# Optimization experiments

Hardware: AMD Instinct MI355X
Metric: run time of the kernel (lower is better)

The kernel has to match this reference:

```python
import jax, jax.numpy as jnp
import numpy as np

N_NODES = 100000
N_EDGES = 1600000
D = 128


def _gconv(x, edge_index, edge_weight, W, Wloop, b):
    # support = x @ W ; out = adj @ support + x @ Wloop + b
    support = x @ W                                   # [N, D]
    src, dst = edge_index[0], edge_index[1]
    msgs = support[src] * edge_weight[:, None]        # [E, D] gather (irregular)
    agg = jax.ops.segment_sum(msgs, dst, num_segments=x.shape[0])  # [N, D] scatter
    return agg + x @ Wloop + b


def setup_inputs() -> dict:
    key = jax.random.key(0)
    ks = jax.random.split(key, 9)
    s = 1.0 / np.sqrt(D)
    x = jax.random.normal(ks[0], (N_NODES, D), dtype=jnp.float32)
    edge_index = jax.random.randint(ks[1], (2, N_EDGES), 0, N_NODES, dtype=jnp.int32)
    edge_weight = jax.random.uniform(ks[2], (N_EDGES,), dtype=jnp.float32)
    W1 = jax.random.normal(ks[3], (D, D), dtype=jnp.float32) * s
    Wloop1 = jax.random.normal(ks[4], (D, D), dtype=jnp.float32) * s
    b1 = jax.random.normal(ks[5], (D,), dtype=jnp.float32) * 0.01
    W2 = jax.random.normal(ks[6], (D, D), dtype=jnp.float32) * s
    Wloop2 = jax.random.normal(ks[7], (D, D), dtype=jnp.float32) * s
    b2 = jax.random.normal(ks[8], (D,), dtype=jnp.float32) * 0.01
    return {"x": x, "edge_index": edge_index, "edge_weight": edge_weight,
            "W1": W1, "Wloop1": Wloop1, "b1": b1,
            "W2": W2, "Wloop2": Wloop2, "b2": b2}


def reference(x, edge_index, edge_weight, W1, Wloop1, b1, W2, Wloop2, b2):
    h = _gconv(x, edge_index, edge_weight, W1, Wloop1, b1)
    h = _gconv(h, edge_index, edge_weight, W2, Wloop2, b2)
    return (x + h) * 0.5
```

## Files before the change

kernel.cpp:

```cpp
#include <hip/hip_runtime.h>
#include <hip/hip_bf16.h>
#include <stdint.h>

#define D 128
#define BM 64
#define NB_BITS 9
#define NPB (1 << NB_BITS)
#define BCAP 10240
#define C3_EPB 4096

typedef __attribute__((ext_vector_type(8))) short bf16x8;
typedef __attribute__((ext_vector_type(4))) short short4_t;
typedef __attribute__((ext_vector_type(4))) float f32x4;
typedef unsigned int uint32;

static __device__ __forceinline__ short f2bf(float f) {
  uint32_t u = __builtin_bit_cast(uint32_t, f);
  u += 0x7fffu + ((u >> 16) & 1u);
  return (short)(u >> 16);
}

static __device__ __forceinline__ uint32 pk2bf(float a, float b) {
  return ((uint32)(unsigned short)f2bf(b) << 16) | (uint32)(unsigned short)f2bf(a);
}


__global__ void k_prep(const float* __restrict__ W1, const float* __restrict__ Wl1,
                       const float* __restrict__ W2, const float* __restrict__ Wl2,
                       short* __restrict__ BT1, short* __restrict__ BT2,
                       int* __restrict__ bcur) {
  int idx = blockIdx.x * 256 + threadIdx.x;
  if (idx < 2 * D * D) {
    int n = idx >> 7, k = idx & (D - 1);
    float v = (n < D) ? W1[k * D + n] : Wl1[k * D + (n - D)];
    BT1[idx] = f2bf(v);
  } else if (idx < 4 * D * D) {
    int i2 = idx - 2 * D * D;
    int n = i2 >> 7, k = i2 & (D - 1);
    float v = (n < D) ? W2[k * D + n] : Wl2[k * D + (n - D)];
    BT2[i2] = f2bf(v);
  } else if (idx < 4 * D * D + 256) {
    bcur[idx - 4 * D * D] = 0;
  }
}


__global__ __launch_bounds__(256) void k_bucket(const int* __restrict__ src,
                                                const int* __restrict__ dst,
                                                const float* __restrict__ wgt,
                                                int* __restrict__ bcur,
                                                int4* __restrict__ rec,
                                                int E, int nb) {
  __shared__ int lhist[256];
  __shared__ int lbase[256];
  const int t = threadIdx.x;
  const int e0 = blockIdx.x * C3_EPB;
  if (t < nb) lhist[t] = 0;
  __syncthreads();
  for (int i = t; i < C3_EPB; i += 256) {
    int e = e0 + i;
    if (e < E) atomicAdd(&lhist[dst[e] >> NB_BITS], 1);
  }
  __syncthreads();
  if (t < nb) {
    lbase[t] = atomicAdd(&bcur[t], lhist[t]);
    lhist[t] = 0;
  }
  __syncthreads();
  for (int i = t; i < C3_EPB; i += 256) {
    int e = e0 + i;
    if (e < E) {
      int d = dst[e];
      int b = d >> NB_BITS;
      int r = lbase[b] + atomicAdd(&lhist[b], 1);
      if (r >= BCAP) r = BCAP - 1;
      rec[(size_t)b * BCAP + r] =
          make_int4(src[e], __builtin_bit_cast(int, wgt[e]), d, 0);
    }
  }
}


__global__ __launch_bounds__(256) void k_sort(const int4* __restrict__ rec,
                                              const int* __restrict__ bcur,
                                              int* __restrict__ off,
                                              int2* __restrict__ pairs,
                                              int N, int nb) {
  __shared__ int bc[256];
  __shared__ int psum[256];
  __shared__ int lofs[NPB];
  const int t = threadIdx.x;
  const int b = blockIdx.x;

  int mycnt = (t < nb) ? min(bcur[t], BCAP) : 0;
  bc[t] = mycnt;
  __syncthreads();
  for (int dd = 1; dd < 256; dd <<= 1) {
    int a = (t >= dd) ? bc[t - dd] : 0;
    __syncthreads();
    bc[t] += a;
    __syncthreads();
  }
  const int cntb = min(bcur[b], BCAP);
  const int ebase = bc[b] - cntb;
  const int total = bc[nb - 1];
  const size_t rbase = (size_t)b * BCAP;
  const int n0 = b << NB_BITS;
  const int nn = min(NPB, N - n0);

  for (int i = t; i < NPB; i += 256) lofs[i] = 0;
  __syncthreads();
  for (int i = t; i < cntb; i += 256)
    atomicAdd(&lofs[rec[rbase + i].z & (NPB - 1)], 1);
  __syncthreads();

  int v0 = lofs[2 * t], v1 = lofs[2 * t + 1];
  int sum = v0 + v1;
  psum[t] = sum;
  __syncthreads();
  for (int dd = 1; dd < 256; dd <<= 1) {
    int a = (t >= dd) ? psum[t - dd] : 0;
    __syncthreads();
    psum[t] += a;
    __syncthreads();
  }
  int run = psum[t] - sum;
  lofs[2 * t] = run;
  lofs[2 * t + 1] = run + v0;
  __syncthreads();

  for (int i = t; i < nn; i += 256) off[n0 + i] = ebase + lofs[i];
  if (b == nb - 1 && t == 0) off[N] = total;
  __syncthreads();

  for (int i = t; i < cntb; i += 256) {
    int4 rr = rec[rbase + i];
    int r = atomicAdd(&lofs[rr.z & (NPB - 1)], 1);
    pairs[ebase + r] = make_int2(rr.x, rr.y);
  }
}


template<bool ABF16, bool IBF16, bool RESID>
__global__ __launch_bounds__(256) void k_gemm(const void* __restrict__ Ap,
                                              const short* __restrict__ BT,
                                              const float* __restrict__ bias,
                                              const float* __restrict__ resid,
                                              unsigned short* __restrict__ support,
                                              void* __restrict__ initp, int M) {
  __shared__ short As[BM * D];
  const int t = threadIdx.x;
  const int l = t & 63;
  const int w = t >> 6;
  const int lm = l & 15;
  const int lg = l >> 4;
  const int m0 = blockIdx.x * BM;
  const bool full = (m0 + BM <= M);

  short4_t aregs[8];
  float4 aregf[8];
#pragma unroll
  for (int i = 0; i < 8; ++i) {
    int id = t + i * 256;
    int row = id >> 5, c4 = id & 31;
    int gr = m0 + row; if (gr >= M) gr = M - 1;
    if (ABF16) aregs[i] = *(const short4_t*)((const short*)Ap + (size_t)gr * D + c4 * 4);
    else       aregf[i] = *(const float4*)((const float*)Ap + (size_t)gr * D + c4 * 4);
  }

  bf16x8 bfrag[4][4];
  const int colbase = w * 64 + lm;
#pragma unroll
  for (int cf = 0; cf < 4; ++cf) {
    const short* p = BT + (colbase + cf * 16) * D + lg * 8;
#pragma unroll
    for (int ks = 0; ks < 4; ++ks) bfrag[cf][ks] = *(const bf16x8*)(p + ks * 32);
  }

#pragma unroll
  for (int i = 0; i < 8; ++i) {
    int id = t + i * 256;
    int row = id >> 5, c4 = id & 31;
    short4_t s4;
    if (ABF16) s4 = aregs[i];
    else {
      float4 v = aregf[i];
      s4[0] = f2bf(v.x); s4[1] = f2bf(v.y); s4[2] = f2bf(v.z); s4[3] = f2bf(v.w);
    }
    int sidx = row * D + ((c4 * 4) ^ ((row & 7) << 3));
    *(short4_t*)(As + sidx) = s4;
  }
  __syncthreads();

  f32x4 acc[4][4] = {};
#pragma unroll
  for (int ks = 0; ks < 4; ++ks) {
    bf16x8 afrag[4];
    int kcol = ks * 32 + lg * 8;
#pragma unroll
    for (int rf = 0; rf < 4; ++rf) {
      int row = rf * 16 + lm;
      afrag[rf] = *(const bf16x8*)(As + row * D + (kcol ^ ((row & 7) << 3)));
    }
#pragma unroll
    for (int rf = 0; rf < 4; ++rf)
#pragma unroll
      for (int cf = 0; cf < 4; ++cf)
        acc[rf][cf] = __builtin_amdgcn_mfma_f32_16x16x32_bf16(
            bfrag[cf][ks], afrag[rf], acc[rf][cf], 0, 0, 0);
  }

  const bool isInit = (w >= 2);
  const int wcol = (w & 1) * 64;

  if (!isInit) {
#pragma unroll
    for (int rf = 0; rf < 4; ++rf) {
      int m = m0 + rf * 16 + lm;
#pragma unroll
      for (int cf = 0; cf < 4; ++cf) {
        int nb = wcol + cf * 16 + lg * 4;
        f32x4 a = acc[rf][cf];
        uint2 pk = make_uint2(pk2bf(a[0], a[1]), pk2bf(a[2], a[3]));
        if (full || m < M)
          *(uint2*)((uint32*)support + (size_t)m * 64 + (nb >> 1)) = pk;
      }
    }
  } else {
    float4 bv4[4];
#pragma unroll
    for (int cf = 0; cf < 4; ++cf)
      bv4[cf] = *(const float4*)(bias + wcol + cf * 16 + lg * 4);
#pragma unroll
    for (int rf = 0; rf < 4; ++rf) {
      int m = m0 + rf * 16 + lm;
      bool ok = full || m < M;
#pragma unroll
      for (int cf = 0; cf < 4; ++cf) {
        int nb = wcol + cf * 16 + lg * 4;
        f32x4 a = acc[rf][cf];
        float4 v;
        v.x = a[0] + bv4[cf].x; v.y = a[1] + bv4[cf].y;
        v.z = a[2] + bv4[cf].z; v.w = a[3] + bv4[cf].w;
        if (RESID) {
          if (ok) {
            float4 xr = *(const float4*)(resid + (size_t)m * D + nb);
            v.x = (v.x + xr.x) * 0.5f; v.y = (v.y + xr.y) * 0.5f;
            v.z = (v.z + xr.z) * 0.5f; v.w = (v.w + xr.w) * 0.5f;
          }
        }
        if (ok) {
          if (IBF16) {
            uint2 pk = make_uint2(pk2bf(v.x, v.y), pk2bf(v.z, v.w));
            *(uint2*)((uint32*)initp + (size_t)m * 64 + (nb >> 1)) = pk;
          } else {
            *(float4*)((float*)initp + (size_t)m * D + nb) = v;
          }
        }
      }
    }
  }
}


template<int MODE>
__global__ __launch_bounds__(256) void k_agg(const uint32* __restrict__ sup,
                                             const int* __restrict__ off,
                                             const int2* __restrict__ pairs,
                                             void* __restrict__ iop, int N) {
  int node = blockIdx.x * 4 + (threadIdx.x >> 6);
  if (node >= N) return;
  const int l = threadIdx.x & 63;
  const int beg = __builtin_amdgcn_readfirstlane(off[node]);
  const int end = __builtin_amdgcn_readfirstlane(off[node + 1]);
  float ax = 0.f, ay = 0.f;
  const int nbt = (end - beg + 7) >> 3;

  if (nbt > 0) {
    int pr[8], pw[8];
#pragma unroll
    for (int i = 0; i < 8; ++i) {
      int jj = beg + i;
      int jc = jj < end ? jj : beg;
      int2 tt = pairs[jc];
      pr[i] = __builtin_amdgcn_readfirstlane(tt.x);
      pw[i] = __builtin_amdgcn_readfirstlane(jj < end ? tt.y : 0);
    }
    int j = beg + 8;
    for (int b = 1; b < nbt; ++b, j += 8) {
      int nr[8], nw[8];
#pragma unroll
      for (int i = 0; i < 8; ++i) {
        int jj = j + i;
        int jc = jj < end ? jj : beg;
        int2 tt = pairs[jc];
        nr[i] = __builtin_amdgcn_readfirstlane(tt.x);
        nw[i] = __builtin_amdgcn_readfirstlane(jj < end ? tt.y : 0);
      }
      uint32 v[8];
#pragma unroll
      for (int i = 0; i < 8; ++i) v[i] = sup[(size_t)(uint32)pr[i] * 64 + l];
#pragma unroll
      for (int i = 0; i < 8; ++i) {
        float w = __builtin_bit_cast(float, pw[i]);
        ax = fmaf(__builtin_bit_cast(float, v[i] << 16), w, ax);
        ay = fmaf(__builtin_bit_cast(float, v[i] & 0xffff0000u), w, ay);
      }
#pragma unroll
      for (int i = 0; i < 8; ++i) { pr[i] = nr[i]; pw[i] = nw[i]; }
    }
    uint32 v[8];
#pragma unroll
    for (int i = 0; i < 8; ++i) v[i] = sup[(size_t)(uint32)pr[i] * 64 + l];
#pragma unroll
    for (int i = 0; i < 8; ++i) {
      float w = __builtin_bit_cast(float, pw[i]);
      ax = fmaf(__builtin_bit_cast(float, v[i] << 16), w, ax);
      ay = fmaf(__builtin_bit_cast(float, v[i] & 0xffff0000u), w, ay);
    }
  }

  size_t o = (size_t)node * 64 + l;
  if (MODE == 0) {
    uint32* io = (uint32*)iop;
    uint32 cur = io[o];
    float vx = __builtin_bit_cast(float, cur << 16) + ax;
    float vy = __builtin_bit_cast(float, cur & 0xffff0000u) + ay;
    io[o] = ((uint32)(unsigned short)f2bf(vy) << 16) | (unsigned short)f2bf(vx);
  } else {
    float2* io = (float2*)iop;
    float2 v = io[o];
    v.x = fmaf(0.5f, ax, v.x);
    v.y = fmaf(0.5f, ay, v.y);
    io[o] = v;
  }
}


extern "C" void kernel_launch(void* const* d_in, const int* in_sizes, int n_in,
                              void* d_out, int out_size, void* d_ws, size_t ws_size,
                              hipStream_t stream) {
  const float* x   = (const float*)d_in[0];
  const int*   ei  = (const int*)d_in[1];
  const float* ew  = (const float*)d_in[2];
  const float* W1  = (const float*)d_in[3];
  const float* Wl1 = (const float*)d_in[4];
  const float* b1  = (const float*)d_in[5];
  const float* W2  = (const float*)d_in[6];
  const float* Wl2 = (const float*)d_in[7];
  const float* b2  = (const float*)d_in[8];
  float* out = (float*)d_out;

  const int N = in_sizes[0] / D;
  const int E = in_sizes[1] / 2;
  const int* src = ei;
  const int* dst = ei + E;
  const int nbuck = (N + NPB - 1) >> NB_BITS;

  uint32* sup = (uint32*)d_ws;
  uint32* h1b = sup + (size_t)N * 64;
  short* BT1  = (short*)(h1b + (size_t)N * 64);
  short* BT2  = BT1 + 2 * D * D;
  int* bcur   = (int*)(BT2 + 2 * D * D);
  int* off    = bcur + 256;
  int2* pairs = (int2*)(off + (N + 4));
  int4* rec   = (int4*)(pairs + E);

  k_prep<<<(4 * D * D + 256 + 255) / 256, 256, 0, stream>>>(W1, Wl1, W2, Wl2, BT1, BT2, bcur);

  k_bucket<<<(E + C3_EPB - 1) / C3_EPB, 256, 0, stream>>>(src, dst, ew, bcur, rec, E, nbuck);
  k_sort<<<nbuck, 256, 0, stream>>>(rec, bcur, off, pairs, N, nbuck);

  const int mblocks = (N + BM - 1) / BM;
  const int ablocks = (N + 3) / 4;

  k_gemm<false, true, false><<<mblocks, 256, 0, stream>>>(
      x, BT1, b1, nullptr, (unsigned short*)sup, h1b, N);
  k_agg<0><<<ablocks, 256, 0, stream>>>(sup, off, pairs, h1b, N);

  k_gemm<true, false, true><<<mblocks, 256, 0, stream>>>(
      h1b, BT2, b2, x, (unsigned short*)sup, out, N);
  k_agg<1><<<ablocks, 256, 0, stream>>>(sup, off, pairs, out, N);
}
```

Before: 268.0 us.

## Reorder layer-2 as aggregate-then-GEMM with concatenated K=256 weights

Layer 2 is reassociated: h1 is aggregated over the edges first (adj@h1), and a single GEMM then multiplies the concatenated [agg|h1] (K=256) by stacked [W2;Wloop2], fusing bias, residual and the 0.5 scale. This removes the layer-2 support write and the fp32 read-modify-write of the output in the aggregation kernel, since aggregation now writes only bf16 partial sums. It reuses the rec buffer for the aggregated tensor and adds LDS use for the wider A tile, plus an extra bf16 rounding of the aggregated values.

```diff
diff --git a/kernel.cpp b/kernel.cpp
--- a/kernel.cpp
+++ b/kernel.cpp
@@ -36,8 +36,8 @@
     BT1[idx] = f2bf(v);
   } else if (idx < 4 * D * D) {
     int i2 = idx - 2 * D * D;
-    int n = i2 >> 7, k = i2 & (D - 1);
-    float v = (n < D) ? W2[k * D + n] : Wl2[k * D + (n - D)];
+    int n = i2 >> 8, k = i2 & 255;
+    float v = (k < D) ? W2[k * D + n] : Wl2[(k - D) * D + n];
     BT2[i2] = f2bf(v);
   } else if (idx < 4 * D * D + 256) {
     bcur[idx - 4 * D * D] = 0;
@@ -141,13 +141,11 @@
 }
 
 
-template<bool ABF16, bool IBF16, bool RESID>
-__global__ __launch_bounds__(256) void k_gemm(const void* __restrict__ Ap,
-                                              const short* __restrict__ BT,
-                                              const float* __restrict__ bias,
-                                              const float* __restrict__ resid,
-                                              unsigned short* __restrict__ support,
-                                              void* __restrict__ initp, int M) {
+__global__ __launch_bounds__(256) void k_gemm1(const float* __restrict__ A,
+                                               const short* __restrict__ BT,
+                                               const float* __restrict__ bias,
+                                               unsigned short* __restrict__ support,
+                                               unsigned short* __restrict__ initp, int M) {
   __shared__ short As[BM * D];
   const int t = threadIdx.x;
   const int l = t & 63;
@@ -157,15 +155,13 @@
   const int m0 = blockIdx.x * BM;
   const bool full = (m0 + BM <= M);
 
-  short4_t aregs[8];
   float4 aregf[8];
 #pragma unroll
   for (int i = 0; i < 8; ++i) {
     int id = t + i * 256;
     int row = id >> 5, c4 = id & 31;
     int gr = m0 + row; if (gr >= M) gr = M - 1;
-    if (ABF16) aregs[i] = *(const short4_t*)((const short*)Ap + (size_t)gr * D + c4 * 4);
-    else       aregf[i] = *(const float4*)((const float*)Ap + (size_t)gr * D + c4 * 4);
+    aregf[i] = *(const float4*)(A + (size_t)gr * D + c4 * 4);
   }
 
   bf16x8 bfrag[4][4];
@@ -181,12 +177,8 @@
   for (int i = 0; i < 8; ++i) {
     int id = t + i * 256;
     int row = id >> 5, c4 = id & 31;
-    short4_t s4;
-    if (ABF16) s4 = aregs[i];
-    else {
-      float4 v = aregf[i];
-      s4[0] = f2bf(v.x); s4[1] = f2bf(v.y); s4[2] = f2bf(v.z); s4[3] = f2bf(v.w);
-    }
+    float4 v = aregf[i];
+    short4_t s4 = { f2bf(v.x), f2bf(v.y), f2bf(v.z), f2bf(v.w) };
     int sidx = row * D + ((c4 * 4) ^ ((row & 7) << 3));
     *(short4_t*)(As + sidx) = s4;
   }
@@ -239,25 +231,92 @@
       for (int cf = 0; cf < 4; ++cf) {
         int nb = wcol + cf * 16 + lg * 4;
         f32x4 a = acc[rf][cf];
-        float4 v;
-        v.x = a[0] + bv4[cf].x; v.y = a[1] + bv4[cf].y;
-        v.z = a[2] + bv4[cf].z; v.w = a[3] + bv4[cf].w;
-        if (RESID) {
-          if (ok) {
-            float4 xr = *(const float4*)(resid + (size_t)m * D + nb);
-            v.x = (v.x + xr.x) * 0.5f; v.y = (v.y + xr.y) * 0.5f;
-            v.z = (v.z + xr.z) * 0.5f; v.w = (v.w + xr.w) * 0.5f;
-          }
-        }
         if (ok) {
-          if (IBF16) {
-            uint2 pk = make_uint2(pk2bf(v.x, v.y), pk2bf(v.z, v.w));
-            *(uint2*)((uint32*)initp + (size_t)m * 64 + (nb >> 1)) = pk;
-          } else {
-            *(float4*)((float*)initp + (size_t)m * D + nb) = v;
-          }
+          uint2 pk = make_uint2(pk2bf(a[0] + bv4[cf].x, a[1] + bv4[cf].y),
+                                pk2bf(a[2] + bv4[cf].z, a[3] + bv4[cf].w));
+          *(uint2*)((uint32*)initp + (size_t)m * 64 + (nb >> 1)) = pk;
         }
       }
+    }
+  }
+}
+
+
+__global__ __launch_bounds__(256) void k_gemm2(const uint32* __restrict__ aggb,
+                                               const uint32* __restrict__ h1b,
+                                               const short* __restrict__ BT,
+                                               const float* __restrict__ bias,
+                                               const float* __restrict__ resid,
+                                               float* __restrict__ out, int M) {
+  __shared__ short As[BM * 256];
+  const int t = threadIdx.x;
+  const int l = t & 63;
+  const int w = t >> 6;
+  const int lm = l & 15;
+  const int lg = l >> 4;
+  const int m0 = blockIdx.x * BM;
+  const bool full = (m0 + BM <= M);
+
+#pragma unroll
+  for (int i = 0; i < 8; ++i) {
+    int id = t + i * 256;
+    int row = id >> 5, c8 = id & 31;
+    int gr = m0 + row; if (gr >= M) gr = M - 1;
+    const uint32* srcp = (c8 < 16) ? (aggb + (size_t)gr * 64 + c8 * 4)
+                                   : (h1b + (size_t)gr * 64 + (c8 - 16) * 4);
+    uint4 v = *(const uint4*)srcp;
+    int sidx = row * 256 + ((c8 * 8) ^ ((row & 7) << 3));
+    *(uint4*)(As + sidx) = v;
+  }
+
+  bf16x8 bfrag[2][8];
+  const int colbase = w * 32 + lm;
+#pragma unroll
+  for (int cf = 0; cf < 2; ++cf) {
+    const short* p = BT + (colbase + cf * 16) * 256 + lg * 8;
+#pragma unroll
+    for (int ks = 0; ks < 8; ++ks) bfrag[cf][ks] = *(const bf16x8*)(p + ks * 32);
+  }
+  __syncthreads();
+
+  f32x4 acc[4][2] = {};
+#pragma unroll
+  for (int ks = 0; ks < 8; ++ks) {
+    bf16x8 afrag[4];
+    int kcol = ks * 32 + lg * 8;
+#pragma unroll
+    for (int rf = 0; rf < 4; ++rf) {
+      int row = rf * 16 + lm;
+      afrag[rf] = *(const bf16x8*)(As + row * 256 + (kcol ^ ((row & 7) << 3)));
+    }
+#pragma unroll
+    for (int rf = 0; rf < 4; ++rf)
+#pragma unroll
+      for (int cf = 0; cf < 2; ++cf)
+        acc[rf][cf] = __builtin_amdgcn_mfma_f32_16x16x32_bf16(
+            bfrag[cf][ks], afrag[rf], acc[rf][cf], 0, 0, 0);
+  }
+
+  float4 bv4[2];
+#pragma unroll
+  for (int cf = 0; cf < 2; ++cf)
+    bv4[cf] = *(const float4*)(bias + w * 32 + cf * 16 + lg * 4);
+#pragma unroll
+  for (int rf = 0; rf < 4; ++rf) {
+    int m = m0 + rf * 16 + lm;
+    bool ok = full || m < M;
+    if (!ok) continue;
+#pragma unroll
+    for (int cf = 0; cf < 2; ++cf) {
+      int nb = w * 32 + cf * 16 + lg * 4;
+      f32x4 a = acc[rf][cf];
+      float4 xr = *(const float4*)(resid + (size_t)m * D + nb);
+      float4 v;
+      v.x = (a[0] + bv4[cf].x + xr.x) * 0.5f;
+      v.y = (a[1] + bv4[cf].y + xr.y) * 0.5f;
+      v.z = (a[2] + bv4[cf].z + xr.z) * 0.5f;
+      v.w = (a[3] + bv4[cf].w + xr.w) * 0.5f;
+      *(float4*)(out + (size_t)m * D + nb) = v;
     }
   }
 }
@@ -267,7 +326,7 @@
 __global__ __launch_bounds__(256) void k_agg(const uint32* __restrict__ sup,
                                              const int* __restrict__ off,
                                              const int2* __restrict__ pairs,
-                                             void* __restrict__ iop, int N) {
+                                             uint32* __restrict__ iop, int N) {
   int node = blockIdx.x * 4 + (threadIdx.x >> 6);
   if (node >= N) return;
   const int l = threadIdx.x & 63;
@@ -322,17 +381,12 @@
 
   size_t o = (size_t)node * 64 + l;
   if (MODE == 0) {
-    uint32* io = (uint32*)iop;
-    uint32 cur = io[o];
+    uint32 cur = iop[o];
     float vx = __builtin_bit_cast(float, cur << 16) + ax;
     float vy = __builtin_bit_cast(float, cur & 0xffff0000u) + ay;
-    io[o] = ((uint32)(unsigned short)f2bf(vy) << 16) | (unsigned short)f2bf(vx);
+    iop[o] = pk2bf(vx, vy);
   } else {
-    float2* io = (float2*)iop;
-    float2 v = io[o];
-    v.x = fmaf(0.5f, ax, v.x);
-    v.y = fmaf(0.5f, ay, v.y);
-    io[o] = v;
+    iop[o] = pk2bf(ax, ay);
   }
 }
 
@@ -365,6 +419,7 @@
   int* off    = bcur + 256;
   int2* pairs = (int2*)(off + (N + 4));
   int4* rec   = (int4*)(pairs + E);
+  uint32* aggb = (uint32*)rec;
 
   k_prep<<<(4 * D * D + 256 + 255) / 256, 256, 0, stream>>>(W1, Wl1, W2, Wl2, BT1, BT2, bcur);
 
@@ -374,11 +429,9 @@
   const int mblocks = (N + BM - 1) / BM;
   const int ablocks = (N + 3) / 4;
 
-  k_gemm<false, true, false><<<mblocks, 256, 0, stream>>>(
-      x, BT1, b1, nullptr, (unsigned short*)sup, h1b, N);
+  k_gemm1<<<mblocks, 256, 0, stream>>>(x, BT1, b1, (unsigned short*)sup, (unsigned short*)h1b, N);
   k_agg<0><<<ablocks, 256, 0, stream>>>(sup, off, pairs, h1b, N);
 
-  k_gemm<true, false, true><<<mblocks, 256, 0, stream>>>(
-      h1b, BT2, b2, x, (unsigned short*)sup, out, N);
-  k_agg<1><<<ablocks, 256, 0, stream>>>(sup, off, pairs, out, N);
-}
+  k_agg<2><<<ablocks, 256, 0, stream>>>(h1b, off, pairs, aggb, N);
+  k_gemm2<<<mblocks, 256, 0, stream>>>(aggb, h1b, BT2, b2, x, out, N);
+}
```

Result: faster. 249.8 us (-6.8%).
